# Kernel tuning notes

Measured on AMD Instinct MI355X. Metric: run time of the kernel, lower is better.

## Reference

```python
import jax, jax.numpy as jnp
import numpy as np

BS, L, D = 4, 2048, 1024
H, E, K = 8, 16, 2
HD = D // H            # 128
I = 4096 // H          # 512 per-expert intermediate


def setup_inputs() -> dict:
    key = jax.random.key(0)
    ks = jax.random.split(key, 10)
    s = lambda k, shp, fan: jax.random.normal(k, shp, jnp.float32) / np.sqrt(fan)
    return {
        "x": jax.random.normal(ks[0], (BS, L, D), jnp.float32),
        "Wm": s(ks[1], (D, D), D),
        "bm": jnp.zeros((D,), jnp.float32),
        "expert_emb": jax.random.normal(ks[2], (HD, E), jnp.float32),
        "W1": s(ks[3], (E, HD, I), HD),
        "b1": jnp.zeros((E, I), jnp.float32),
        "W2": s(ks[4], (E, I, HD), I),
        "b2": jnp.zeros((E, HD), jnp.float32),
        "Wo": s(ks[5], (D, D), D),
        "bo": jnp.zeros((D,), jnp.float32),
    }


def reference(x, Wm, bm, expert_emb, W1, b1, W2, b2, Wo, bo):
    bs, L_, d = x.shape
    # multi_head projection then split each token into H sub-tokens of HD dims
    h = x @ Wm + bm                              # [bs, L, d]
    t = h.reshape(bs * L_ * H, HD)               # [T, HD], T = bs*L*H
    # routing per sub-token
    logits = t @ expert_emb                      # [T, E]
    w = jax.nn.softmax(logits, axis=-1)
    topw, topi = jax.lax.top_k(w, K)             # [T, K]
    # dense all-experts MLP (faithful to torch.stack over all experts)
    hmid = jax.nn.gelu(jnp.einsum('td,edi->tei', t, W1) + b1, approximate=False)  # [T, E, I]
    eo = jnp.einsum('tei,eio->teo', hmid, W2) + b2                                # [T, E, HD]
    # gather top-k expert outputs and combine with router weights
    sel = jnp.take_along_axis(eo, topi[:, :, None], axis=1)   # [T, K, HD]
    comb = (sel * topw[:, :, None]).sum(axis=1)               # [T, HD]
    out = comb.reshape(bs, L_, d)
    return out @ Wo + bo
```

## Files before the change

kernel.cpp:

```cpp
#include <hip/hip_runtime.h>
#include <hip/hip_bf16.h>
#include <math.h>

typedef __attribute__((ext_vector_type(8))) short bx8;
typedef __attribute__((ext_vector_type(4))) short sx4;
typedef __attribute__((ext_vector_type(4))) float fx4;

#define D_   1024
#define H_   8
#define E_   16
#define HD_  128
#define I_   512
#define M8_  8192
#define T_   65536

__device__ inline float bf2f(short u) {
  unsigned int x = ((unsigned int)(unsigned short)u) << 16;
  return __builtin_bit_cast(float, x);
}
__device__ inline short f2bf(float f) {
  __hip_bfloat16 h = __float2bfloat16(f);
  return __builtin_bit_cast(short, h);
}

__device__ inline void gload_lds16(const void* g, void* l) {
  __builtin_amdgcn_global_load_lds(
      (const __attribute__((address_space(1))) void*)g,
      (__attribute__((address_space(3))) void*)l, 16, 0, 0);
}

__device__ inline fx4 mfma16(bx8 a, bx8 b, fx4 c) {
  return __builtin_amdgcn_mfma_f32_16x16x32_bf16(a, b, c, 0, 0, 0);
}

__device__ inline float gelu_erf(float x) {
  float z = fabsf(x) * 0.70710678118654752f;
  float t = __builtin_amdgcn_rcpf(fmaf(0.3275911f, z, 1.f));
  float p = t * fmaf(t, fmaf(t, fmaf(t, fmaf(t, 1.061405429f, -1.453152027f),
                                     1.421413741f), -0.284496736f), 0.254829592f);
  float er = fmaf(-p, __expf(-z * z), 1.f);
  er = copysignf(er, x);
  return 0.5f * x * (1.f + er);
}


__global__ __launch_bounds__(256) void cvt_bf16_k(const float* __restrict__ src,
                                                  __hip_bfloat16* __restrict__ dst) {
  int i = blockIdx.x * 256 + threadIdx.x;
  float4 v = *(const float4*)&src[(size_t)i * 4];
  sx4 o;
  o[0] = f2bf(v.x); o[1] = f2bf(v.y); o[2] = f2bf(v.z); o[3] = f2bf(v.w);
  *(sx4*)((short*)dst + (size_t)i * 4) = o;
}

__global__ __launch_bounds__(256) void tcvt(const float* __restrict__ src,
                                            __hip_bfloat16* __restrict__ dst,
                                            int R, int C) {
  __shared__ float tile[32][33];
  int tx = threadIdx.x & 31, ty = threadIdx.x >> 5;
  int r0 = blockIdx.y * 32, c0 = blockIdx.x * 32;
  const float* s = src + (size_t)blockIdx.z * R * C;
  __hip_bfloat16* d = dst + (size_t)blockIdx.z * R * C;
#pragma unroll
  for (int i = ty; i < 32; i += 8) tile[i][tx] = s[(size_t)(r0 + i) * C + c0 + tx];
  __syncthreads();
#pragma unroll
  for (int i = ty; i < 32; i += 8)
    d[(size_t)(c0 + i) * R + r0 + tx] = __float2bfloat16(tile[tx][i]);
}


__global__ __launch_bounds__(128) void build_wre(const float* __restrict__ Wm,
                                                 const float* __restrict__ bm,
                                                 const float* __restrict__ emb,
                                                 float* __restrict__ Wre,
                                                 float* __restrict__ rbias) {
  __shared__ float wrow[1024];
  __shared__ float embs[2048];
  int tid = threadIdx.x;
  int d = blockIdx.x;
  for (int i = tid; i < 2048; i += 128) embs[i] = emb[i];
  for (int i = tid; i < 1024; i += 128) wrow[i] = Wm[(size_t)d * 1024 + i];
  __syncthreads();
  int eta = tid >> 4, e = tid & 15;
  float acc = 0.f;
  for (int c = 0; c < 128; ++c) acc = fmaf(wrow[eta * 128 + c], embs[c * 16 + e], acc);
  Wre[(size_t)d * 128 + tid] = acc;
  if (blockIdx.x == 0) {
    float b = 0.f;
    for (int c = 0; c < 128; ++c) b = fmaf(bm[eta * 128 + c], embs[c * 16 + e], b);
    rbias[tid] = b;
  }
}

__global__ __launch_bounds__(256) void route_fused(const float* __restrict__ x,
                                                   const float* __restrict__ Wre,
                                                   const float* __restrict__ rbias,
                                                   float* __restrict__ topw,
                                                   int* __restrict__ list,
                                                   int* __restrict__ cnt) {
  __shared__ float xs[16][64];
  __shared__ float wsh[64][128];
  __shared__ float ls[16][129];
  __shared__ int lcnt[16];
  __shared__ int gbase[16];
  int tid = threadIdx.x;
  int n = tid & 127, half = tid >> 7;
  int row0 = blockIdx.x * 16;
  if (tid < 16) lcnt[tid] = 0;
  float acc[8];
#pragma unroll
  for (int i = 0; i < 8; ++i) acc[i] = 0.f;

  for (int k0 = 0; k0 < 1024; k0 += 64) {
    __syncthreads();
    {
      int i4 = tid * 4;
      int row = i4 >> 6, col = i4 & 63;
      *(float4*)&xs[row][col] = *(const float4*)&x[(size_t)(row0 + row) * 1024 + k0 + col];
    }
#pragma unroll
    for (int j = 0; j < 8; ++j) {
      int i4 = tid * 4 + j * 1024;
      int row = i4 >> 7, col = i4 & 127;
      *(float4*)&wsh[row][col] = *(const float4*)&Wre[(size_t)(k0 + row) * 128 + col];
    }
    __syncthreads();
#pragma unroll 4
    for (int d4 = 0; d4 < 64; d4 += 4) {
      float w0 = wsh[d4 + 0][n], w1 = wsh[d4 + 1][n];
      float w2 = wsh[d4 + 2][n], w3 = wsh[d4 + 3][n];
#pragma unroll
      for (int i = 0; i < 8; ++i) {
        float4 xv = *(const float4*)&xs[half * 8 + i][d4];
        acc[i] = fmaf(xv.x, w0, acc[i]);
        acc[i] = fmaf(xv.y, w1, acc[i]);
        acc[i] = fmaf(xv.z, w2, acc[i]);
        acc[i] = fmaf(xv.w, w3, acc[i]);
      }
    }
  }
  float rb = rbias[n];
#pragma unroll
  for (int i = 0; i < 8; ++i) ls[half * 8 + i][n] = acc[i] + rb;
  __syncthreads();

  int i1 = 0, i2 = 0, lp1 = 0, lp2 = 0, s = 0;
  if (tid < 128) {
    int lr = tid >> 3, eta = tid & 7;
    s = (row0 + lr) * 8 + eta;
    float v[16];
#pragma unroll
    for (int e = 0; e < 16; ++e) v[e] = ls[lr][eta * 16 + e];
    float v1 = -1e30f, v2 = -1e30f;
#pragma unroll
    for (int e = 0; e < 16; ++e) {
      float val = v[e];
      if (val > v1) { v2 = v1; i2 = i1; v1 = val; i1 = e; }
      else if (val > v2) { v2 = val; i2 = e; }
    }
    float sum = 0.f;
#pragma unroll
    for (int e = 0; e < 16; ++e) sum += expf(v[e] - v1);
    topw[(size_t)2 * s + 0] = 1.0f / sum;
    topw[(size_t)2 * s + 1] = expf(v2 - v1) / sum;
    lp1 = atomicAdd(&lcnt[i1], 1);
    lp2 = atomicAdd(&lcnt[i2], 1);
  }
  __syncthreads();
  if (tid < 16) gbase[tid] = atomicAdd(&cnt[tid], lcnt[tid]);
  __syncthreads();
  if (tid < 128) {
    list[(size_t)i1 * T_ + gbase[i1] + lp1] = 2 * s;
    list[(size_t)i2 * T_ + gbase[i2] + lp2] = 2 * s + 1;
  }
}

__global__ void prefix_k(const int* __restrict__ cnt, int* __restrict__ tileBase) {
  if (threadIdx.x == 0 && blockIdx.x == 0) {
    int s = 0;
#pragma unroll
    for (int e = 0; e < 16; ++e) { tileBase[e] = s; s += (cnt[e] + 63) >> 6; }
    tileBase[16] = s;
  }
}


template <int OUTF32>
__global__ __launch_bounds__(256) void gemm_bt(const __hip_bfloat16* __restrict__ A,
                                               const __hip_bfloat16* __restrict__ BT,
                                               const float* __restrict__ bias,
                                               void* __restrict__ Cout,
                                               int M, int N, int Kd) {
  __shared__ __hip_bfloat16 As[128 * 64];
  __shared__ __hip_bfloat16 Bs[128 * 64];
  int tid = threadIdx.x;
  int lane = tid & 63, w = tid >> 6;
  int nbn = N >> 7;
  int cpx = gridDim.x >> 3;
  int swz = (blockIdx.x & 7) * cpx + (blockIdx.x >> 3);
  int bm = swz / nbn, bn = swz % nbn;
  int wm = w >> 1, wn = w & 1;
  int r = lane & 15, g = lane >> 4;
  const fx4 fz = {0.f, 0.f, 0.f, 0.f};
  fx4 acc[4][4];
#pragma unroll
  for (int m = 0; m < 4; ++m)
#pragma unroll
    for (int n = 0; n < 4; ++n) acc[m][n] = fz;
  const short* AsS = (const short*)As;
  const short* BsS = (const short*)Bs;
  for (int k0 = 0; k0 < Kd; k0 += 64) {
    __syncthreads();
#pragma unroll
    for (int i = 0; i < 4; ++i) {
      int c = i * 256 + w * 64 + lane;
      int row = c >> 3, ko = (c & 7) * 8;
      gload_lds16(A + (size_t)(bm * 128 + row) * Kd + k0 + ko,
                  (void*)(As + (size_t)(i * 256 + w * 64) * 8));
    }
#pragma unroll
    for (int i = 0; i < 4; ++i) {
      int c = i * 256 + w * 64 + lane;
      int row = c >> 3, ko = (c & 7) * 8;
      gload_lds16(BT + (size_t)(bn * 128 + row) * Kd + k0 + ko,
                  (void*)(Bs + (size_t)(i * 256 + w * 64) * 8));
    }
    __syncthreads();
#pragma unroll
    for (int kb = 0; kb < 2; ++kb) {
      bx8 af[4], bfr[4];
#pragma unroll
      for (int m = 0; m < 4; ++m)
        af[m] = *(const bx8*)(AsS + (wm * 64 + m * 16 + r) * 64 + kb * 32 + g * 8);
#pragma unroll
      for (int n = 0; n < 4; ++n)
        bfr[n] = *(const bx8*)(BsS + (wn * 64 + n * 16 + r) * 64 + kb * 32 + g * 8);
#pragma unroll
      for (int m = 0; m < 4; ++m)
#pragma unroll
        for (int n = 0; n < 4; ++n)
          acc[m][n] = mfma16(af[m], bfr[n], acc[m][n]);
    }
  }
#pragma unroll
  for (int n = 0; n < 4; ++n) {
    int col = bn * 128 + wn * 64 + n * 16 + r;
    float bv = bias[col];
#pragma unroll
    for (int m = 0; m < 4; ++m) {
      int rowb = bm * 128 + wm * 64 + m * 16 + g * 4;
#pragma unroll
      for (int ri = 0; ri < 4; ++ri) {
        float val = acc[m][n][ri] + bv;
        if (OUTF32) ((float*)Cout)[(size_t)(rowb + ri) * N + col] = val;
        else ((__hip_bfloat16*)Cout)[(size_t)(rowb + ri) * N + col] = __float2bfloat16(val);
      }
    }
  }
}


__global__ __launch_bounds__(256, 4) void expert_mlp3(
    const __hip_bfloat16* __restrict__ h,
    const __hip_bfloat16* __restrict__ W1T,
    const __hip_bfloat16* __restrict__ W2T,
    const float* __restrict__ b1,
    const float* __restrict__ b2,
    const float* __restrict__ topw,
    const int* __restrict__ list,
    const int* __restrict__ cnt,
    const int* __restrict__ tileBase,
    __hip_bfloat16* __restrict__ eo) {
  int b = blockIdx.x;
  if (b >= tileBase[16]) return;
  int e = 0;
#pragma unroll
  for (int i = 1; i < 16; ++i) e += (b >= tileBase[i]);
  int tile = b - tileBase[e];
  int cnt_e = cnt[e];
  int base = tile * 64;
  if (base >= cnt_e) return;

  __shared__ short W1c[64 * 128];
  __shared__ short W2c[128 * 64];
  __shared__ short Hc[4 * 16 * 64];

  int tid = threadIdx.x, lane = tid & 63, wv = tid >> 6;
  int r = lane & 15, g = lane >> 4;
  const int* liste = list + (size_t)e * T_;

  int idx_own = base + wv * 16 + r;
  int p_own = (idx_own < cnt_e) ? liste[idx_own] : -1;
  const short* hS = (const short*)h;
  size_t st = (p_own >= 0) ? (size_t)(p_own >> 1) : 0;
  const short* rp = hS + st * 128 + g * 8;
  bx8 af[4];
#pragma unroll
  for (int kb = 0; kb < 4; ++kb) af[kb] = *(const bx8*)(rp + kb * 32);

  const char* W1S = (const char*)(W1T + (size_t)e * I_ * HD_);
  const char* W2S = (const char*)(W2T + (size_t)e * HD_ * I_);
  const float* b1e = b1 + (size_t)e * I_;
  const float* b2e = b2 + (size_t)e * HD_;
  char* HcW = (char*)Hc + wv * 16 * 128;

  const fx4 fz = {0.f, 0.f, 0.f, 0.f};
  fx4 acc2[8];
#pragma unroll
  for (int n = 0; n < 8; ++n) acc2[n] = fz;

  for (int c = 0; c < 8; ++c) {
    __syncthreads();
#pragma unroll
    for (int j = 0; j < 4; ++j) {
      int row = wv * 16 + j * 4 + (lane >> 4);
      int u = lane & 15;
      gload_lds16(W1S + (size_t)(c * 64 + row) * 256 + ((u * 16) ^ ((row & 7) << 4)),
                  (char*)W1c + (wv * 16 + j * 4) * 256);
    }
#pragma unroll
    for (int j = 0; j < 4; ++j) {
      int row = wv * 32 + j * 8 + (lane >> 3);
      int u = lane & 7;
      gload_lds16(W2S + (size_t)row * 1024 + c * 128 + ((u * 16) ^ ((row & 7) << 4)),
                  (char*)W2c + (wv * 32 + j * 8) * 128);
    }
    __syncthreads();

    fx4 acc1[4];
#pragma unroll
    for (int ib = 0; ib < 4; ++ib) acc1[ib] = fz;
#pragma unroll
    for (int kb = 0; kb < 4; ++kb) {
#pragma unroll
      for (int ib = 0; ib < 4; ++ib) {
        int irow = ib * 16 + r;
        bx8 a = *(const bx8*)((const char*)W1c + irow * 256 +
                              ((kb * 64 + g * 16) ^ ((irow & 7) << 4)));
        acc1[ib] = mfma16(a, af[kb], acc1[ib]);
      }
    }

#pragma unroll
    for (int ib = 0; ib < 4; ++ib) {
      float4 b1v = *(const float4*)&b1e[c * 64 + ib * 16 + g * 4];
      sx4 ov;
      ov[0] = f2bf(gelu_erf(acc1[ib][0] + b1v.x));
      ov[1] = f2bf(gelu_erf(acc1[ib][1] + b1v.y));
      ov[2] = f2bf(gelu_erf(acc1[ib][2] + b1v.z));
      ov[3] = f2bf(gelu_erf(acc1[ib][3] + b1v.w));
      *(sx4*)(HcW + r * 128 + ((ib * 32 + g * 8) ^ ((r & 7) << 4))) = ov;
    }

#pragma unroll
    for (int kb2 = 0; kb2 < 2; ++kb2) {
      bx8 ha = *(const bx8*)(HcW + r * 128 + ((kb2 * 64 + g * 16) ^ ((r & 7) << 4)));
#pragma unroll
      for (int ob = 0; ob < 8; ++ob) {
        int orow = ob * 16 + r;
        bx8 wb = *(const bx8*)((const char*)W2c + orow * 128 +
                               ((kb2 * 64 + g * 16) ^ ((orow & 7) << 4)));
        acc2[ob] = mfma16(ha, wb, acc2[ob]);
      }
    }
  }

  int pid_ep[4];
  float wt_ep[4];
#pragma unroll
  for (int ri = 0; ri < 4; ++ri) {
    int idx = base + wv * 16 + g * 4 + ri;
    int p = (idx < cnt_e) ? liste[idx] : -1;
    pid_ep[ri] = p;
    wt_ep[ri] = (p >= 0) ? topw[p] : 0.f;
  }
#pragma unroll
  for (int ob = 0; ob < 8; ++ob) {
    float b2v = b2e[ob * 16 + r];
#pragma unroll
    for (int ri = 0; ri < 4; ++ri) {
      int p = pid_ep[ri];
      if (p >= 0) {
        float v = (acc2[ob][ri] + b2v) * wt_ep[ri];
        eo[(size_t)p * 128 + ob * 16 + r] = __float2bfloat16(v);
      }
    }
  }
}

__global__ __launch_bounds__(256) void combine_k(const __hip_bfloat16* __restrict__ eo,
                                                 __hip_bfloat16* __restrict__ comb) {
  int t = blockIdx.x * 256 + threadIdx.x;
  int s = t >> 4, oo = (t & 15) * 8;
  const short* eS = (const short*)eo;
  bx8 a = *(const bx8*)(eS + (size_t)s * 256 + oo);
  bx8 b = *(const bx8*)(eS + (size_t)s * 256 + 128 + oo);
  bx8 ov;
#pragma unroll
  for (int j = 0; j < 8; ++j) ov[j] = f2bf(bf2f(a[j]) + bf2f(b[j]));
  *(bx8*)((short*)comb + (size_t)s * 128 + oo) = ov;
}


extern "C" void kernel_launch(void* const* d_in, const int* in_sizes, int n_in,
                              void* d_out, int out_size, void* d_ws, size_t ws_size,
                              hipStream_t stream) {
  const float* x   = (const float*)d_in[0];
  const float* Wm  = (const float*)d_in[1];
  const float* bm  = (const float*)d_in[2];
  const float* emb = (const float*)d_in[3];
  const float* W1  = (const float*)d_in[4];
  const float* b1  = (const float*)d_in[5];
  const float* W2  = (const float*)d_in[6];
  const float* b2  = (const float*)d_in[7];
  const float* Wo  = (const float*)d_in[8];
  const float* bo  = (const float*)d_in[9];

  char* ws = (char*)d_ws;
  size_t off = 0;
  auto alloc = [&](size_t b) { size_t r = off; off += (b + 255) & ~(size_t)255; return r; };
  __hip_bfloat16* xb   = (__hip_bfloat16*)(ws + alloc((size_t)M8_ * D_ * 2));
  __hip_bfloat16* WmT  = (__hip_bfloat16*)(ws + alloc((size_t)D_ * D_ * 2));
  __hip_bfloat16* WoT  = (__hip_bfloat16*)(ws + alloc((size_t)D_ * D_ * 2));
  __hip_bfloat16* W1T  = (__hip_bfloat16*)(ws + alloc((size_t)E_ * HD_ * I_ * 2));
  __hip_bfloat16* W2T  = (__hip_bfloat16*)(ws + alloc((size_t)E_ * HD_ * I_ * 2));
  __hip_bfloat16* hb   = (__hip_bfloat16*)(ws + alloc((size_t)M8_ * D_ * 2));
  float* Wre    = (float*)(ws + alloc((size_t)D_ * 128 * 4));
  float* rbias  = (float*)(ws + alloc(512));
  float* topw   = (float*)(ws + alloc((size_t)T_ * 2 * 4));
  int*   cnt    = (int*)(ws + alloc(256));
  int*   tileBase = (int*)(ws + alloc(256));
  int*   list   = (int*)(ws + alloc((size_t)E_ * T_ * 4));
  __hip_bfloat16* eo   = (__hip_bfloat16*)(ws + alloc((size_t)T_ * 2 * HD_ * 2));
  __hip_bfloat16* comb = (__hip_bfloat16*)(ws + alloc((size_t)M8_ * D_ * 2));

  hipMemsetAsync(cnt, 0, 256, stream);
  cvt_bf16_k<<<8192, 256, 0, stream>>>(x, xb);
  tcvt<<<dim3(32, 32, 1), 256, 0, stream>>>(Wm, WmT, 1024, 1024);
  tcvt<<<dim3(32, 32, 1), 256, 0, stream>>>(Wo, WoT, 1024, 1024);
  tcvt<<<dim3(16, 4, 16), 256, 0, stream>>>(W1, W1T, 128, 512);
  tcvt<<<dim3(4, 16, 16), 256, 0, stream>>>(W2, W2T, 512, 128);
  build_wre<<<1024, 128, 0, stream>>>(Wm, bm, emb, Wre, rbias);
  gemm_bt<0><<<512, 256, 0, stream>>>(xb, WmT, bm, hb, M8_, D_, D_);
  route_fused<<<512, 256, 0, stream>>>(x, Wre, rbias, topw, list, cnt);
  prefix_k<<<1, 32, 0, stream>>>(cnt, tileBase);
  expert_mlp3<<<2064, 256, 0, stream>>>(hb, W1T, W2T, b1, b2, topw, list, cnt,
                                        tileBase, eo);
  combine_k<<<4096, 256, 0, stream>>>(eo, comb);
  gemm_bt<1><<<512, 256, 0, stream>>>(comb, WoT, bo, d_out, M8_, D_, D_);
}
```

Measured before the change: 362.0 us.

## Double expert MLP tile to 128 rows, double-buffer W1, fuse x bf16 conversion into routing

The expert MLP kernel now processes 128 routed sub-tokens per block, two 16-row m-tiles per wave. This halves the number of blocks and reuses each staged W1/W2 chunk across twice as many rows, and W1 chunks are double-buffered so the next load overlaps compute. The standalone fp32-to-bf16 conversion of x is folded into the routing kernel, which already reads x, and the routing weight matrix is stored transposed so LDS reads vectorise. In exchange the kernel uses more registers and LDS (occupancy hint lowered to 2), adds extra barriers per chunk, and the early exit for empty tiles is removed.

```diff
diff --git a/kernel.cpp b/kernel.cpp
--- a/kernel.cpp
+++ b/kernel.cpp
@@ -44,15 +44,6 @@
 }
 
 
-__global__ __launch_bounds__(256) void cvt_bf16_k(const float* __restrict__ src,
-                                                  __hip_bfloat16* __restrict__ dst) {
-  int i = blockIdx.x * 256 + threadIdx.x;
-  float4 v = *(const float4*)&src[(size_t)i * 4];
-  sx4 o;
-  o[0] = f2bf(v.x); o[1] = f2bf(v.y); o[2] = f2bf(v.z); o[3] = f2bf(v.w);
-  *(sx4*)((short*)dst + (size_t)i * 4) = o;
-}
-
 __global__ __launch_bounds__(256) void tcvt(const float* __restrict__ src,
                                             __hip_bfloat16* __restrict__ dst,
                                             int R, int C) {
@@ -73,7 +64,7 @@
 __global__ __launch_bounds__(128) void build_wre(const float* __restrict__ Wm,
                                                  const float* __restrict__ bm,
                                                  const float* __restrict__ emb,
-                                                 float* __restrict__ Wre,
+                                                 float* __restrict__ WreT,
                                                  float* __restrict__ rbias) {
   __shared__ float wrow[1024];
   __shared__ float embs[2048];
@@ -85,7 +76,7 @@
   int eta = tid >> 4, e = tid & 15;
   float acc = 0.f;
   for (int c = 0; c < 128; ++c) acc = fmaf(wrow[eta * 128 + c], embs[c * 16 + e], acc);
-  Wre[(size_t)d * 128 + tid] = acc;
+  WreT[(size_t)tid * 1024 + d] = acc;
   if (blockIdx.x == 0) {
     float b = 0.f;
     for (int c = 0; c < 128; ++c) b = fmaf(bm[eta * 128 + c], embs[c * 16 + e], b);
@@ -93,56 +84,68 @@
   }
 }
 
-__global__ __launch_bounds__(256) void route_fused(const float* __restrict__ x,
-                                                   const float* __restrict__ Wre,
-                                                   const float* __restrict__ rbias,
-                                                   float* __restrict__ topw,
-                                                   int* __restrict__ list,
-                                                   int* __restrict__ cnt) {
+__global__ __launch_bounds__(256) void route_fused2(const float* __restrict__ x,
+                                                    const float* __restrict__ WreT,
+                                                    const float* __restrict__ rbias,
+                                                    __hip_bfloat16* __restrict__ xb,
+                                                    float* __restrict__ topw,
+                                                    int* __restrict__ list,
+                                                    int* __restrict__ cnt) {
   __shared__ float xs[16][64];
-  __shared__ float wsh[64][128];
+  __shared__ float wshT[128][68];
   __shared__ float ls[16][129];
   __shared__ int lcnt[16];
   __shared__ int gbase[16];
   int tid = threadIdx.x;
-  int n = tid & 127, half = tid >> 7;
+  int rg = tid >> 6, cg = tid & 63;
   int row0 = blockIdx.x * 16;
   if (tid < 16) lcnt[tid] = 0;
-  float acc[8];
-#pragma unroll
-  for (int i = 0; i < 8; ++i) acc[i] = 0.f;
+  float acc[4][2];
+#pragma unroll
+  for (int i = 0; i < 4; ++i) { acc[i][0] = 0.f; acc[i][1] = 0.f; }
 
   for (int k0 = 0; k0 < 1024; k0 += 64) {
     __syncthreads();
     {
       int i4 = tid * 4;
       int row = i4 >> 6, col = i4 & 63;
-      *(float4*)&xs[row][col] = *(const float4*)&x[(size_t)(row0 + row) * 1024 + k0 + col];
+      float4 xv = *(const float4*)&x[(size_t)(row0 + row) * 1024 + k0 + col];
+      *(float4*)&xs[row][col] = xv;
+      sx4 o;
+      o[0] = f2bf(xv.x); o[1] = f2bf(xv.y); o[2] = f2bf(xv.z); o[3] = f2bf(xv.w);
+      *(sx4*)((short*)xb + (size_t)(row0 + row) * 1024 + k0 + col) = o;
     }
 #pragma unroll
     for (int j = 0; j < 8; ++j) {
-      int i4 = tid * 4 + j * 1024;
-      int row = i4 >> 7, col = i4 & 127;
-      *(float4*)&wsh[row][col] = *(const float4*)&Wre[(size_t)(k0 + row) * 128 + col];
+      int idx = tid + j * 256;
+      int n = idx >> 4, kq = (idx & 15) * 4;
+      *(float4*)&wshT[n][kq] = *(const float4*)&WreT[(size_t)n * 1024 + k0 + kq];
     }
     __syncthreads();
 #pragma unroll 4
     for (int d4 = 0; d4 < 64; d4 += 4) {
-      float w0 = wsh[d4 + 0][n], w1 = wsh[d4 + 1][n];
-      float w2 = wsh[d4 + 2][n], w3 = wsh[d4 + 3][n];
-#pragma unroll
-      for (int i = 0; i < 8; ++i) {
-        float4 xv = *(const float4*)&xs[half * 8 + i][d4];
-        acc[i] = fmaf(xv.x, w0, acc[i]);
-        acc[i] = fmaf(xv.y, w1, acc[i]);
-        acc[i] = fmaf(xv.z, w2, acc[i]);
-        acc[i] = fmaf(xv.w, w3, acc[i]);
-      }
-    }
-  }
-  float rb = rbias[n];
-#pragma unroll
-  for (int i = 0; i < 8; ++i) ls[half * 8 + i][n] = acc[i] + rb;
+      float4 w0 = *(const float4*)&wshT[cg][d4];
+      float4 w1 = *(const float4*)&wshT[cg + 64][d4];
+#pragma unroll
+      for (int rr = 0; rr < 4; ++rr) {
+        float4 xv = *(const float4*)&xs[rg * 4 + rr][d4];
+        acc[rr][0] = fmaf(xv.x, w0.x, acc[rr][0]);
+        acc[rr][0] = fmaf(xv.y, w0.y, acc[rr][0]);
+        acc[rr][0] = fmaf(xv.z, w0.z, acc[rr][0]);
+        acc[rr][0] = fmaf(xv.w, w0.w, acc[rr][0]);
+        acc[rr][1] = fmaf(xv.x, w1.x, acc[rr][1]);
+        acc[rr][1] = fmaf(xv.y, w1.y, acc[rr][1]);
+        acc[rr][1] = fmaf(xv.z, w1.z, acc[rr][1]);
+        acc[rr][1] = fmaf(xv.w, w1.w, acc[rr][1]);
+      }
+    }
+  }
+  float rb0 = rbias[cg], rb1 = rbias[cg + 64];
+#pragma unroll
+  for (int rr = 0; rr < 4; ++rr) {
+    ls[rg * 4 + rr][cg] = acc[rr][0] + rb0;
+    ls[rg * 4 + rr][cg + 64] = acc[rr][1] + rb1;
+  }
   __syncthreads();
 
   int i1 = 0, i2 = 0, lp1 = 0, lp2 = 0, s = 0;
@@ -180,7 +183,7 @@
   if (threadIdx.x == 0 && blockIdx.x == 0) {
     int s = 0;
 #pragma unroll
-    for (int e = 0; e < 16; ++e) { tileBase[e] = s; s += (cnt[e] + 63) >> 6; }
+    for (int e = 0; e < 16; ++e) { tileBase[e] = s; s += (cnt[e] + 127) >> 7; }
     tileBase[16] = s;
   }
 }
@@ -261,7 +264,7 @@
 }
 
 
-__global__ __launch_bounds__(256, 4) void expert_mlp3(
+__global__ __launch_bounds__(256, 2) void expert_mlp4(
     const __hip_bfloat16* __restrict__ h,
     const __hip_bfloat16* __restrict__ W1T,
     const __hip_bfloat16* __restrict__ W2T,
@@ -279,46 +282,43 @@
   for (int i = 1; i < 16; ++i) e += (b >= tileBase[i]);
   int tile = b - tileBase[e];
   int cnt_e = cnt[e];
-  int base = tile * 64;
-  if (base >= cnt_e) return;
-
-  __shared__ short W1c[64 * 128];
+  int base = tile * 128;
+
+  __shared__ short W1c[2][64 * 128];
   __shared__ short W2c[128 * 64];
-  __shared__ short Hc[4 * 16 * 64];
+  __shared__ short Hc[4][32 * 64];
 
   int tid = threadIdx.x, lane = tid & 63, wv = tid >> 6;
   int r = lane & 15, g = lane >> 4;
   const int* liste = list + (size_t)e * T_;
-
-  int idx_own = base + wv * 16 + r;
-  int p_own = (idx_own < cnt_e) ? liste[idx_own] : -1;
   const short* hS = (const short*)h;
-  size_t st = (p_own >= 0) ? (size_t)(p_own >> 1) : 0;
-  const short* rp = hS + st * 128 + g * 8;
-  bx8 af[4];
-#pragma unroll
-  for (int kb = 0; kb < 4; ++kb) af[kb] = *(const bx8*)(rp + kb * 32);
+
+  bx8 af[2][4];
+#pragma unroll
+  for (int tm = 0; tm < 2; ++tm) {
+    int idx = base + wv * 32 + tm * 16 + r;
+    int p = (idx < cnt_e) ? liste[idx] : -1;
+    const short* rp = hS + (size_t)((p >= 0) ? (p >> 1) : 0) * 128 + g * 8;
+#pragma unroll
+    for (int kb = 0; kb < 4; ++kb) af[tm][kb] = *(const bx8*)(rp + kb * 32);
+  }
 
   const char* W1S = (const char*)(W1T + (size_t)e * I_ * HD_);
   const char* W2S = (const char*)(W2T + (size_t)e * HD_ * I_);
   const float* b1e = b1 + (size_t)e * I_;
   const float* b2e = b2 + (size_t)e * HD_;
-  char* HcW = (char*)Hc + wv * 16 * 128;
-
-  const fx4 fz = {0.f, 0.f, 0.f, 0.f};
-  fx4 acc2[8];
-#pragma unroll
-  for (int n = 0; n < 8; ++n) acc2[n] = fz;
-
-  for (int c = 0; c < 8; ++c) {
-    __syncthreads();
+  char* HcW = (char*)Hc[wv];
+
+  auto stageW1 = [&](int buf, int c) {
 #pragma unroll
     for (int j = 0; j < 4; ++j) {
       int row = wv * 16 + j * 4 + (lane >> 4);
       int u = lane & 15;
       gload_lds16(W1S + (size_t)(c * 64 + row) * 256 + ((u * 16) ^ ((row & 7) << 4)),
-                  (char*)W1c + (wv * 16 + j * 4) * 256);
-    }
+                  (char*)W1c[buf] + (wv * 16 + j * 4) * 256);
+    }
+  };
+  auto stageW2 = [&](int c) {
 #pragma unroll
     for (int j = 0; j < 4; ++j) {
       int row = wv * 32 + j * 8 + (lane >> 3);
@@ -326,64 +326,91 @@
       gload_lds16(W2S + (size_t)row * 1024 + c * 128 + ((u * 16) ^ ((row & 7) << 4)),
                   (char*)W2c + (wv * 32 + j * 8) * 128);
     }
-    __syncthreads();
-
-    fx4 acc1[4];
-#pragma unroll
-    for (int ib = 0; ib < 4; ++ib) acc1[ib] = fz;
+  };
+
+  const fx4 fz = {0.f, 0.f, 0.f, 0.f};
+  fx4 acc2[2][8];
+#pragma unroll
+  for (int tm = 0; tm < 2; ++tm)
+#pragma unroll
+    for (int n = 0; n < 8; ++n) acc2[tm][n] = fz;
+
+  stageW1(0, 0);
+  __syncthreads();
+
+  for (int c = 0; c < 8; ++c) {
+    int cur = c & 1;
+    stageW2(c);
+    if (c < 7) stageW1(cur ^ 1, c + 1);
+
+    fx4 acc1[4][2];
+#pragma unroll
+    for (int ib = 0; ib < 4; ++ib) { acc1[ib][0] = fz; acc1[ib][1] = fz; }
 #pragma unroll
     for (int kb = 0; kb < 4; ++kb) {
 #pragma unroll
       for (int ib = 0; ib < 4; ++ib) {
         int irow = ib * 16 + r;
-        bx8 a = *(const bx8*)((const char*)W1c + irow * 256 +
-                              ((kb * 64 + g * 16) ^ ((irow & 7) << 4)));
-        acc1[ib] = mfma16(a, af[kb], acc1[ib]);
+        bx8 a = *(const bx8*)((const char*)W1c[cur] + irow * 256 +
+                              ((kb * 64 + g * 16) ^ ((r & 7) << 4)));
+        acc1[ib][0] = mfma16(a, af[0][kb], acc1[ib][0]);
+        acc1[ib][1] = mfma16(a, af[1][kb], acc1[ib][1]);
       }
     }
 
 #pragma unroll
     for (int ib = 0; ib < 4; ++ib) {
       float4 b1v = *(const float4*)&b1e[c * 64 + ib * 16 + g * 4];
-      sx4 ov;
-      ov[0] = f2bf(gelu_erf(acc1[ib][0] + b1v.x));
-      ov[1] = f2bf(gelu_erf(acc1[ib][1] + b1v.y));
-      ov[2] = f2bf(gelu_erf(acc1[ib][2] + b1v.z));
-      ov[3] = f2bf(gelu_erf(acc1[ib][3] + b1v.w));
-      *(sx4*)(HcW + r * 128 + ((ib * 32 + g * 8) ^ ((r & 7) << 4))) = ov;
-    }
+#pragma unroll
+      for (int tm = 0; tm < 2; ++tm) {
+        sx4 ov;
+        ov[0] = f2bf(gelu_erf(acc1[ib][tm][0] + b1v.x));
+        ov[1] = f2bf(gelu_erf(acc1[ib][tm][1] + b1v.y));
+        ov[2] = f2bf(gelu_erf(acc1[ib][tm][2] + b1v.z));
+        ov[3] = f2bf(gelu_erf(acc1[ib][tm][3] + b1v.w));
+        int t = tm * 16 + r;
+        *(sx4*)(HcW + t * 128 + ((ib * 32 + g * 8) ^ ((r & 7) << 4))) = ov;
+      }
+    }
+
+    __syncthreads();
 
 #pragma unroll
     for (int kb2 = 0; kb2 < 2; ++kb2) {
-      bx8 ha = *(const bx8*)(HcW + r * 128 + ((kb2 * 64 + g * 16) ^ ((r & 7) << 4)));
+      bx8 ha0 = *(const bx8*)(HcW + r * 128 + ((kb2 * 64 + g * 16) ^ ((r & 7) << 4)));
+      bx8 ha1 = *(const bx8*)(HcW + (16 + r) * 128 + ((kb2 * 64 + g * 16) ^ ((r & 7) << 4)));
 #pragma unroll
       for (int ob = 0; ob < 8; ++ob) {
-        int orow = ob * 16 + r;
-        bx8 wb = *(const bx8*)((const char*)W2c + orow * 128 +
-                               ((kb2 * 64 + g * 16) ^ ((orow & 7) << 4)));
-        acc2[ob] = mfma16(ha, wb, acc2[ob]);
-      }
-    }
-  }
-
-  int pid_ep[4];
-  float wt_ep[4];
-#pragma unroll
-  for (int ri = 0; ri < 4; ++ri) {
-    int idx = base + wv * 16 + g * 4 + ri;
-    int p = (idx < cnt_e) ? liste[idx] : -1;
-    pid_ep[ri] = p;
-    wt_ep[ri] = (p >= 0) ? topw[p] : 0.f;
-  }
-#pragma unroll
-  for (int ob = 0; ob < 8; ++ob) {
-    float b2v = b2e[ob * 16 + r];
+        bx8 wb = *(const bx8*)((const char*)W2c + (ob * 16 + r) * 128 +
+                               ((kb2 * 64 + g * 16) ^ ((r & 7) << 4)));
+        acc2[0][ob] = mfma16(ha0, wb, acc2[0][ob]);
+        acc2[1][ob] = mfma16(ha1, wb, acc2[1][ob]);
+      }
+    }
+    __syncthreads();
+  }
+
+#pragma unroll
+  for (int tm = 0; tm < 2; ++tm) {
+    int pid_ep[4];
+    float wt_ep[4];
 #pragma unroll
     for (int ri = 0; ri < 4; ++ri) {
-      int p = pid_ep[ri];
-      if (p >= 0) {
-        float v = (acc2[ob][ri] + b2v) * wt_ep[ri];
-        eo[(size_t)p * 128 + ob * 16 + r] = __float2bfloat16(v);
+      int idx = base + wv * 32 + tm * 16 + g * 4 + ri;
+      int p = (idx < cnt_e) ? liste[idx] : -1;
+      pid_ep[ri] = p;
+      wt_ep[ri] = (p >= 0) ? topw[p] : 0.f;
+    }
+#pragma unroll
+    for (int ob = 0; ob < 8; ++ob) {
+      float b2v = b2e[ob * 16 + r];
+#pragma unroll
+      for (int ri = 0; ri < 4; ++ri) {
+        int p = pid_ep[ri];
+        if (p >= 0) {
+          float v = (acc2[tm][ob][ri] + b2v) * wt_ep[ri];
+          eo[(size_t)p * 128 + ob * 16 + r] = __float2bfloat16(v);
+        }
       }
     }
   }
@@ -426,7 +453,7 @@
   __hip_bfloat16* W1T  = (__hip_bfloat16*)(ws + alloc((size_t)E_ * HD_ * I_ * 2));
   __hip_bfloat16* W2T  = (__hip_bfloat16*)(ws + alloc((size_t)E_ * HD_ * I_ * 2));
   __hip_bfloat16* hb   = (__hip_bfloat16*)(ws + alloc((size_t)M8_ * D_ * 2));
-  float* Wre    = (float*)(ws + alloc((size_t)D_ * 128 * 4));
+  float* WreT   = (float*)(ws + alloc((size_t)128 * D_ * 4));
   float* rbias  = (float*)(ws + alloc(512));
   float* topw   = (float*)(ws + alloc((size_t)T_ * 2 * 4));
   int*   cnt    = (int*)(ws + alloc(256));
@@ -436,16 +463,15 @@
   __hip_bfloat16* comb = (__hip_bfloat16*)(ws + alloc((size_t)M8_ * D_ * 2));
 
   hipMemsetAsync(cnt, 0, 256, stream);
-  cvt_bf16_k<<<8192, 256, 0, stream>>>(x, xb);
   tcvt<<<dim3(32, 32, 1), 256, 0, stream>>>(Wm, WmT, 1024, 1024);
   tcvt<<<dim3(32, 32, 1), 256, 0, stream>>>(Wo, WoT, 1024, 1024);
   tcvt<<<dim3(16, 4, 16), 256, 0, stream>>>(W1, W1T, 128, 512);
   tcvt<<<dim3(4, 16, 16), 256, 0, stream>>>(W2, W2T, 512, 128);
-  build_wre<<<1024, 128, 0, stream>>>(Wm, bm, emb, Wre, rbias);
+  build_wre<<<1024, 128, 0, stream>>>(Wm, bm, emb, WreT, rbias);
+  route_fused2<<<512, 256, 0, stream>>>(x, WreT, rbias, xb, topw, list, cnt);
+  prefix_k<<<1, 32, 0, stream>>>(cnt, tileBase);
   gemm_bt<0><<<512, 256, 0, stream>>>(xb, WmT, bm, hb, M8_, D_, D_);
-  route_fused<<<512, 256, 0, stream>>>(x, Wre, rbias, topw, list, cnt);
-  prefix_k<<<1, 32, 0, stream>>>(cnt, tileBase);
-  expert_mlp3<<<2064, 256, 0, stream>>>(hb, W1T, W2T, b1, b2, topw, list, cnt,
+  expert_mlp4<<<1040, 256, 0, stream>>>(hb, W1T, W2T, b1, b2, topw, list, cnt,
                                         tileBase, eo);
   combine_k<<<4096, 256, 0, stream>>>(eo, comb);
   gemm_bt<1><<<512, 256, 0, stream>>>(comb, WoT, bo, d_out, M8_, D_, D_);
```

Result: slower. 369.8 us (+2.2%).
